# Optimization experiments

Hardware: AMD Instinct MI355X
Metric: run time of the kernel (lower is better)

## Reference

```python
import jax, jax.numpy as jnp
import numpy as np
from functools import partial

INPUT_DIM = 256
HIDDEN = 512
NUM_LAYERS = 2

def _linp(key, fan_in, shape):
    # torch nn.Linear/Conv default init: U(-1/sqrt(fan_in), 1/sqrt(fan_in))
    bound = 1.0 / np.sqrt(fan_in)
    return jax.random.uniform(key, shape, jnp.float32, -bound, bound)

def setup_inputs() -> dict:
    key = jax.random.key(0)
    ks = iter(jax.random.split(key, 64))
    d = {}
    d["x"] = jax.random.normal(next(ks), (32, 16, 1, 64, 64), jnp.float32)
    # encoder convs (OIHW)
    d["conv1_w"] = _linp(next(ks), 1 * 9, (16, 1, 3, 3));   d["conv1_b"] = _linp(next(ks), 1 * 9, (16,))
    d["conv2_w"] = _linp(next(ks), 16 * 9, (32, 16, 3, 3)); d["conv2_b"] = _linp(next(ks), 16 * 9, (32,))
    d["conv3_w"] = _linp(next(ks), 32 * 9, (INPUT_DIM, 32, 3, 3)); d["conv3_b"] = _linp(next(ks), 32 * 9, (INPUT_DIM,))
    # LSTM cells: per layer 4 gate linears (forget, input, cell, output), in = input+hidden
    for j in range(NUM_LAYERS):
        fan = (INPUT_DIM if j == 0 else HIDDEN) + HIDDEN
        for g in ("f", "i", "g", "o"):
            d[f"W{g}{j}"] = _linp(next(ks), fan, (fan, HIDDEN))
            d[f"b{g}{j}"] = _linp(next(ks), fan, (HIDDEN,))
    # classifier
    d["cw1"] = _linp(next(ks), HIDDEN, (HIDDEN, 128)); d["cb1"] = _linp(next(ks), HIDDEN, (128,))
    d["cw2"] = _linp(next(ks), 128, (128, 64));        d["cb2"] = _linp(next(ks), 128, (64,))
    d["cw3"] = _linp(next(ks), 64, (64, 6));           d["cb3"] = _linp(next(ks), 64, (6,))
    return d

def _conv(x, w, b):
    y = jax.lax.conv_general_dilated(x, w, (1, 1), "SAME",
                                     dimension_numbers=("NCHW", "OIHW", "NCHW"))
    return y + b[None, :, None, None]

def _maxpool2(x):
    return jax.lax.reduce_window(x, -jnp.inf, jax.lax.max,
                                 (1, 1, 2, 2), (1, 1, 2, 2), "VALID")

def reference(x, conv1_w, conv1_b, conv2_w, conv2_b, conv3_w, conv3_b,
              Wf0, bf0, Wi0, bi0, Wg0, bg0, Wo0, bo0,
              Wf1, bf1, Wi1, bi1, Wg1, bg1, Wo1, bo1,
              cw1, cb1, cw2, cb2, cw3, cb3):
    B, T, C, H, W = x.shape
    xf = x.reshape(B * T, C, H, W)
    h = _maxpool2(jax.nn.relu(_conv(xf, conv1_w, conv1_b)))
    h = _maxpool2(jax.nn.relu(_conv(h, conv2_w, conv2_b)))
    h = jax.nn.relu(_conv(h, conv3_w, conv3_b))
    emb = h.mean(axis=(2, 3)).reshape(B, T, -1)  # AdaptiveAvgPool2d((1,1)); dropout = identity (eval)

    layers = [(Wf0, bf0, Wi0, bi0, Wg0, bg0, Wo0, bo0),
              (Wf1, bf1, Wi1, bi1, Wg1, bg1, Wo1, bo1)]

    def step(carry, x_t):
        hs, cs = carry
        inp = x_t
        new_h, new_c = [], []
        for j, (Wf, bf, Wi, bi, Wg, bg, Wo, bo) in enumerate(layers):
            comb = jnp.concatenate([inp, hs[j]], axis=1)  # [B, in+H]
            f_t = jax.nn.sigmoid(comb @ Wf + bf)
            i_t = jax.nn.sigmoid(comb @ Wi + bi)
            g_t = jnp.tanh(comb @ Wg + bg)
            o_t = jax.nn.sigmoid(comb @ Wo + bo)
            c_n = f_t * cs[j] + i_t * g_t
            h_n = o_t * jnp.tanh(c_n)
            new_h.append(h_n); new_c.append(c_n)
            inp = h_n
        return (tuple(new_h), tuple(new_c)), None

    h0 = tuple(jnp.zeros((B, HIDDEN), x.dtype) for _ in range(NUM_LAYERS))
    c0 = tuple(jnp.zeros((B, HIDDEN), x.dtype) for _ in range(NUM_LAYERS))
    (hs, _), _ = jax.lax.scan(step, (h0, c0), jnp.swapaxes(emb, 0, 1))
    last = hs[-1]  # [B, HIDDEN], last timestep top-layer h (dropout = identity)

    y = jax.nn.relu(last @ cw1 + cb1)
    y = jax.nn.relu(y @ cw2 + cb2)
    return y @ cw3 + cb3  # [B, 6]
```

## Files before the change

### kernel.cpp

```cpp
#include <hip/hip_runtime.h>
#include <math.h>

__global__ void k_conv1(const float* __restrict__ x, const float* __restrict__ w,
                        const float* __restrict__ bias, float* __restrict__ out) {
  int idx = blockIdx.x * 256 + threadIdx.x;
  int ox = idx & 31, oy = (idx >> 5) & 31, oc = (idx >> 10) & 15, n = idx >> 14;
  const float* im = x + n * 4096;
  float wv[9];
#pragma unroll
  for (int i = 0; i < 9; ++i) wv[i] = w[oc * 9 + i];
  float bs = bias[oc];
  float m = 0.f;
#pragma unroll
  for (int dy = 0; dy < 2; ++dy)
#pragma unroll
    for (int dx = 0; dx < 2; ++dx) {
      int cy = oy * 2 + dy, cx = ox * 2 + dx;
      float s = bs;
#pragma unroll
      for (int ky = 0; ky < 3; ++ky) {
        int yy = cy + ky - 1;
        if (yy < 0 || yy >= 64) continue;
#pragma unroll
        for (int kx = 0; kx < 3; ++kx) {
          int xx = cx + kx - 1;
          if (xx < 0 || xx >= 64) continue;
          s += im[yy * 64 + xx] * wv[ky * 3 + kx];
        }
      }
      m = fmaxf(m, fmaxf(s, 0.f));
    }
  out[idx] = m;
}

__global__ void k_prep_w(const float* __restrict__ w2, float* __restrict__ w2t,
                         const float* __restrict__ w3, float* __restrict__ w3t) {
  int id = blockIdx.x * 256 + threadIdx.x;
  if (id < 73728) {
    int ct = id >> 8, oc = id & 255;
    int c = ct / 9, tap = ct - 9 * c;
    w3t[id] = w3[(oc * 32 + c) * 9 + tap];
  }
  if (id < 4608) {
    int ct = id >> 5, oc = id & 31;
    int c = ct / 9, tap = ct - 9 * c;
    w2t[id] = w2[(oc * 16 + c) * 9 + tap];
  }
}

__global__ __launch_bounds__(256) void k_conv2(
    const float* __restrict__ a1, const float* __restrict__ w2t,
    const float* __restrict__ bias, float* __restrict__ a2) {
  __shared__ __align__(16) float ins[8 * 1024];
  int n = blockIdx.x, ocg = blockIdx.y;
  int tid = threadIdx.x;
  int py = tid >> 4, px = tid & 15;
  int y0 = 2 * py - 1, x0 = 2 * px - 1;
  float acc[16][4] = {};
  const float* wb = w2t + ocg * 16;
  for (int ph = 0; ph < 2; ++ph) {
    __syncthreads();
    const float4* src = (const float4*)(a1 + n * 16384 + ph * 8192);
    for (int i = tid; i < 2048; i += 256) ((float4*)ins)[i] = src[i];
    __syncthreads();
    for (int c = 0; c < 8; ++c) {
      float wv[4][4];
#pragma unroll
      for (int r = 0; r < 4; ++r) {
        int y = y0 + r;
        bool vy = (y >= 0) && (y < 32);
        int yc = vy ? y : 0;
#pragma unroll
        for (int cc = 0; cc < 4; ++cc) {
          int xx = x0 + cc;
          bool vx = (xx >= 0) && (xx < 32);
          int xc = vx ? xx : 0;
          float t = ins[c * 1024 + yc * 32 + xc];
          wv[r][cc] = (vy && vx) ? t : 0.f;
        }
      }
      int ch = ph * 8 + c;
#pragma unroll
      for (int ky = 0; ky < 3; ++ky)
#pragma unroll
        for (int kx = 0; kx < 3; ++kx) {
          const float* w16 = wb + (ch * 9 + ky * 3 + kx) * 32;
#pragma unroll
          for (int i = 0; i < 4; ++i) {
            float vv = wv[(i >> 1) + ky][(i & 1) + kx];
#pragma unroll
            for (int j = 0; j < 16; ++j) acc[j][i] += vv * w16[j];
          }
        }
    }
  }
  const float* bp = bias + ocg * 16;
  float4 o[4];
#pragma unroll
  for (int j = 0; j < 16; ++j) {
    float m = fmaxf(fmaxf(acc[j][0], acc[j][1]), fmaxf(acc[j][2], acc[j][3]));
    ((float*)o)[j] = fmaxf(m + bp[j], 0.f);
  }
  float4* dst = (float4*)(a2 + (size_t)(n * 256 + tid) * 32 + ocg * 16);
#pragma unroll
  for (int q = 0; q < 4; ++q) dst[q] = o[q];
}

__global__ __launch_bounds__(512, 4) void k_conv3(
    const float* __restrict__ a2, const float* __restrict__ w3t,
    const float* __restrict__ bias, float* __restrict__ comb0) {
  __shared__ __align__(16) float ins[324 * 20];
  float4* ins4 = (float4*)ins;
  int n = blockIdx.x, ocb = blockIdx.y;
  int tid = threadIdx.x;
  for (int i = tid; i < 1620; i += 512) ins4[i] = float4{0.f, 0.f, 0.f, 0.f};
  int wvid = __builtin_amdgcn_readfirstlane(tid >> 6);
  int lane = tid & 63;
  int tr = lane >> 4, tc = lane & 15;
  float acc[4][16] = {};
  const float* wbase = w3t + ocb * 128 + wvid * 16;
  const float4* src = (const float4*)(a2 + (size_t)n * 8192);
  for (int hf = 0; hf < 2; ++hf) {
    __syncthreads();
    for (int i = tid; i < 1024; i += 512) {
      int px = i >> 2, cg = i & 3;
      int p = ((px >> 4) + 1) * 18 + (px & 15) + 1;
      ins4[p * 5 + cg] = src[px * 8 + hf * 4 + cg];
    }
    __syncthreads();
    for (int cg = 0; cg < 4; ++cg) {
      int chb = hf * 16 + cg * 4;
#pragma unroll
      for (int dr = 0; dr < 6; ++dr) {
#pragma unroll
        for (int dc = 0; dc < 3; ++dc) {
          int pp = (4 * tr + dr) * 18 + tc + dc;
          float4 v = ins4[pp * 5 + cg];
#pragma unroll
          for (int c = 0; c < 4; ++c) {
            float vv = ((const float*)&v)[c];
            const int ilo = (dr - 2 < 0) ? 0 : dr - 2;
            const int ihi = (dr < 3) ? dr : 3;
#pragma unroll
            for (int i = ilo; i <= ihi; ++i) {
              const float* w16 = wbase + (((chb + c) * 9 + (dr - i) * 3 + dc) * 256);
#pragma unroll
              for (int j = 0; j < 16; ++j) acc[i][j] += vv * w16[j];
            }
          }
        }
      }
    }
  }
  const float* bp = bias + ocb * 128 + wvid * 16;
  int bb = n >> 4, tt = n & 15;
#pragma unroll
  for (int j = 0; j < 16; ++j) {
    float bj = bp[j];
    float s = 0.f;
#pragma unroll
    for (int i = 0; i < 4; ++i) s += fmaxf(acc[i][j] + bj, 0.f);
#pragma unroll
    for (int off = 32; off; off >>= 1) s += __shfl_down(s, off, 64);
    if (lane == 0) {
      int oc = ocb * 128 + wvid * 16 + j;
      comb0[(size_t)(tt * 768 + oc) * 32 + bb] = s * (1.f / 256.f);
    }
  }
}

struct TPtrs { const float* in[8]; float* out[8]; };

__global__ void k_transpose(TPtrs p) {
  __shared__ float tile[32][33];
  int z = blockIdx.z;
  int fan = (z < 4) ? 768 : 1024;
  int k0 = blockIdx.x * 32, h0 = blockIdx.y * 32;
  if (k0 >= fan) return;
  const float* in = p.in[z];
  float* out = p.out[z];
  int tx = threadIdx.x, ty = threadIdx.y;
  for (int r = 0; r < 32; r += 8)
    tile[ty + r][tx] = in[(k0 + ty + r) * 512 + h0 + tx];
  __syncthreads();
  for (int r = 0; r < 32; r += 8)
    out[(h0 + ty + r) * fan + k0 + tx] = tile[tx][ty + r];
}

struct LstmArgs {
  const float* comb; float* houtA; float* houtB; float* cT;
  const float* Wf; const float* Wi; const float* Wg; const float* Wo;
  const float* bf; const float* bi; const float* bg; const float* bo;
};

template <int IN>
__device__ __forceinline__ void lstm_body(int h, int tid, const LstmArgs& A,
                                          float* wl, float* gsum, float* pre) {
  constexpr int FAN = IN + 512;
  constexpr int PR = FAN + 4;
  constexpr int KT = FAN / 16;
  if (tid < FAN / 4) {
    ((float4*)(wl + 0 * PR))[tid] = ((const float4*)(A.Wf + (size_t)h * FAN))[tid];
    ((float4*)(wl + 1 * PR))[tid] = ((const float4*)(A.Wi + (size_t)h * FAN))[tid];
    ((float4*)(wl + 2 * PR))[tid] = ((const float4*)(A.Wg + (size_t)h * FAN))[tid];
    ((float4*)(wl + 3 * PR))[tid] = ((const float4*)(A.Wo + (size_t)h * FAN))[tid];
  }
  __syncthreads();
  const int kq = (tid >> 3) & 15, c = tid >> 7, bq = tid & 7;
  const int kbase = kq * KT;
  const float4* w4 = (const float4*)(wl + c * PR + kbase);
  const float4* a4 = (const float4*)A.comb + bq;
  float acc0 = 0.f, acc1 = 0.f, acc2 = 0.f, acc3 = 0.f;
#pragma unroll
  for (int kk = 0; kk < KT / 4; ++kk) {
    float4 w = w4[kk];
#pragma unroll
    for (int j = 0; j < 4; ++j) {
      float wj = ((const float*)&w)[j];
      float4 a = a4[(size_t)(kbase + kk * 4 + j) * 8];
      acc0 += wj * a.x; acc1 += wj * a.y; acc2 += wj * a.z; acc3 += wj * a.w;
    }
  }
  ((float4*)(gsum + (c * 16 + kq) * 36))[bq] = float4{acc0, acc1, acc2, acc3};
  __syncthreads();
  if (tid < 128) {
    int cc = tid >> 5, b = tid & 31;
    float s = 0.f;
#pragma unroll
    for (int q = 0; q < 16; ++q) s += gsum[(cc * 16 + q) * 36 + b];
    pre[cc * 33 + b] = s;
  }
  __syncthreads();
  if (tid < 32) {
    int b = tid;
    float fp = pre[0 * 33 + b] + A.bf[h];
    float ip = pre[1 * 33 + b] + A.bi[h];
    float gp = pre[2 * 33 + b] + A.bg[h];
    float op = pre[3 * 33 + b] + A.bo[h];
    float ft = 1.f / (1.f + expf(-fp));
    float it = 1.f / (1.f + expf(-ip));
    float gt = tanhf(gp);
    float ot = 1.f / (1.f + expf(-op));
    float cn = ft * A.cT[h * 32 + b] + it * gt;
    A.cT[h * 32 + b] = cn;
    float hn = ot * tanhf(cn);
    A.houtA[h * 32 + b] = hn;
    A.houtB[h * 32 + b] = hn;
  }
}

template <int IN>
__global__ __launch_bounds__(512) void k_lstm(LstmArgs a) {
  __shared__ __align__(16) float wl[4 * 1028];
  __shared__ __align__(16) float gsum[4 * 16 * 36];
  __shared__ float pre[4 * 33];
  lstm_body<IN>(blockIdx.x, threadIdx.x, a, wl, gsum, pre);
}

__global__ __launch_bounds__(512) void k_lstm_pair(LstmArgs a0, LstmArgs a1) {
  __shared__ __align__(16) float wl[4 * 1028];
  __shared__ __align__(16) float gsum[4 * 16 * 36];
  __shared__ float pre[4 * 33];
  if (blockIdx.x < 512)
    lstm_body<256>(blockIdx.x, threadIdx.x, a0, wl, gsum, pre);
  else
    lstm_body<512>(blockIdx.x - 512, threadIdx.x, a1, wl, gsum, pre);
}

__global__ void k_cls(const float* __restrict__ h1T, const float* __restrict__ cw1,
                      const float* __restrict__ cb1, const float* __restrict__ cw2,
                      const float* __restrict__ cb2, const float* __restrict__ cw3,
                      const float* __restrict__ cb3, float* __restrict__ out) {
  __shared__ float hv[512];
  __shared__ float y1[128];
  __shared__ float y2[64];
  int b = blockIdx.x, tid = threadIdx.x;
  for (int i = tid; i < 512; i += 128) hv[i] = h1T[i * 32 + b];
  __syncthreads();
  float s = cb1[tid];
  for (int k = 0; k < 512; ++k) s += hv[k] * cw1[k * 128 + tid];
  y1[tid] = fmaxf(s, 0.f);
  __syncthreads();
  if (tid < 64) {
    float s2 = cb2[tid];
    for (int k = 0; k < 128; ++k) s2 += y1[k] * cw2[k * 64 + tid];
    y2[tid] = fmaxf(s2, 0.f);
  }
  __syncthreads();
  if (tid < 6) {
    float s3 = cb3[tid];
    for (int k = 0; k < 64; ++k) s3 += y2[k] * cw3[k * 6 + tid];
    out[b * 6 + tid] = s3;
  }
}

extern "C" void kernel_launch(void* const* d_in, const int* in_sizes, int n_in,
                              void* d_out, int out_size, void* d_ws, size_t ws_size,
                              hipStream_t stream) {
  const float* x  = (const float*)d_in[0];
  const float* w1 = (const float*)d_in[1];
  const float* b1 = (const float*)d_in[2];
  const float* w2 = (const float*)d_in[3];
  const float* b2 = (const float*)d_in[4];
  const float* w3 = (const float*)d_in[5];
  const float* b3 = (const float*)d_in[6];
  const float* cw1 = (const float*)d_in[23];
  const float* cb1 = (const float*)d_in[24];
  const float* cw2 = (const float*)d_in[25];
  const float* cb2 = (const float*)d_in[26];
  const float* cw3 = (const float*)d_in[27];
  const float* cb3 = (const float*)d_in[28];

  float* ws = (float*)d_ws;
  float* a1    = ws;
  float* wt    = ws;
  float* comb0 = ws + 3670016;
  float* comb1 = ws + 4087808;
  float* c0    = ws + 4644864;
  float* c1    = ws + 4661248;
  float* a2    = ws + 8388608;
  float* w2t   = ws + 12582912;
  float* w3t   = ws + 12587520;
  const int C0 = 768 * 32, C1 = 1024 * 32;

  k_prep_w<<<288, 256, 0, stream>>>(w2, w2t, w3, w3t);
  k_conv1<<<32768, 256, 0, stream>>>(x, w1, b1, a1);
  k_conv2<<<dim3(512, 2), 256, 0, stream>>>(a1, w2t, b2, a2);

  hipMemsetAsync(comb0 + 256 * 32, 0, (size_t)512 * 32 * 4, stream);
  hipMemsetAsync(comb1 + 512 * 32, 0, (size_t)512 * 32 * 4, stream);
  hipMemsetAsync(c0, 0, (size_t)2 * 512 * 32 * 4, stream);

  k_conv3<<<dim3(512, 2), 512, 0, stream>>>(a2, w3t, b3, comb0);

  TPtrs tp;
  for (int g = 0; g < 4; ++g) {
    tp.in[g]      = (const float*)d_in[7 + 2 * g];
    tp.out[g]     = wt + g * (512 * 768);
    tp.in[4 + g]  = (const float*)d_in[15 + 2 * g];
    tp.out[4 + g] = wt + 4 * (512 * 768) + g * (512 * 1024);
  }
  k_transpose<<<dim3(32, 16, 8), dim3(32, 8), 0, stream>>>(tp);

  const float* wl0[4] = {wt, wt + 393216, wt + 786432, wt + 1179648};
  float* l1base = wt + 1572864;
  const float* wl1[4] = {l1base, l1base + 524288, l1base + 1048576, l1base + 1572864};

  auto L0 = [&](int t) {
    LstmArgs a;
    a.comb = comb0 + (size_t)t * C0;
    a.houtA = comb0 + (size_t)(t + 1) * C0 + 256 * 32;
    a.houtB = comb1 + (size_t)t * C1;
    a.cT = c0;
    a.Wf = wl0[0]; a.Wi = wl0[1]; a.Wg = wl0[2]; a.Wo = wl0[3];
    a.bf = (const float*)d_in[8];  a.bi = (const float*)d_in[10];
    a.bg = (const float*)d_in[12]; a.bo = (const float*)d_in[14];
    return a;
  };
  auto L1 = [&](int t) {
    LstmArgs a;
    a.comb = comb1 + (size_t)t * C1;
    a.houtA = comb1 + (size_t)(t + 1) * C1 + 512 * 32;
    a.houtB = a.houtA;
    a.cT = c1;
    a.Wf = wl1[0]; a.Wi = wl1[1]; a.Wg = wl1[2]; a.Wo = wl1[3];
    a.bf = (const float*)d_in[16]; a.bi = (const float*)d_in[18];
    a.bg = (const float*)d_in[20]; a.bo = (const float*)d_in[22];
    return a;
  };

  k_lstm<256><<<512, 512, 0, stream>>>(L0(0));
  for (int p = 0; p < 15; ++p)
    k_lstm_pair<<<1024, 512, 0, stream>>>(L0(p + 1), L1(p));
  k_lstm<512><<<512, 512, 0, stream>>>(L1(15));

  k_cls<<<32, 128, 0, stream>>>(comb1 + (size_t)16 * C1 + 512 * 32,
                                cw1, cb1, cw2, cb2, cw3, cb3, (float*)d_out);
}
```

Before: 687.6 us.

## Retile conv3 to 8 channels per wave and pack LSTM gate weights interleaved

conv3 now runs 256-thread blocks with 8 output channels per wave across 8 channel-block groups. It preloads an 6x3 float4 input window into registers and loops over kernel taps, in place of the earlier per-row accumulate pattern. The LSTM gate weights are packed into one interleaved float4 layout (f,i,g,o per k), so each step kernel streams weights straight from global memory without staging them in LDS. Each wave then reduces a K-slice for all 32 batch lanes with a cross-half shuffle. This aims to cut shared-memory staging and synchronisation per LSTM step and to raise conv3 occupancy, at the cost of more redundant input loads across the extra conv3 blocks.

```diff
diff --git a/kernel.cpp b/kernel.cpp
--- a/kernel.cpp
+++ b/kernel.cpp
@@ -106,56 +106,54 @@
   for (int q = 0; q < 4; ++q) dst[q] = o[q];
 }
 
-__global__ __launch_bounds__(512, 4) void k_conv3(
+__global__ __launch_bounds__(256) void k_conv3(
     const float* __restrict__ a2, const float* __restrict__ w3t,
     const float* __restrict__ bias, float* __restrict__ comb0) {
   __shared__ __align__(16) float ins[324 * 20];
-  float4* ins4 = (float4*)ins;
   int n = blockIdx.x, ocb = blockIdx.y;
   int tid = threadIdx.x;
-  for (int i = tid; i < 1620; i += 512) ins4[i] = float4{0.f, 0.f, 0.f, 0.f};
+  for (int i = tid; i < 1620; i += 256) ((float4*)ins)[i] = float4{0.f, 0.f, 0.f, 0.f};
   int wvid = __builtin_amdgcn_readfirstlane(tid >> 6);
   int lane = tid & 63;
   int tr = lane >> 4, tc = lane & 15;
-  float acc[4][16] = {};
-  const float* wbase = w3t + ocb * 128 + wvid * 16;
+  float acc[4][8] = {};
+  const float* wbase = w3t + ocb * 32 + wvid * 8;
   const float4* src = (const float4*)(a2 + (size_t)n * 8192);
   for (int hf = 0; hf < 2; ++hf) {
     __syncthreads();
-    for (int i = tid; i < 1024; i += 512) {
+    for (int i = tid; i < 1024; i += 256) {
       int px = i >> 2, cg = i & 3;
       int p = ((px >> 4) + 1) * 18 + (px & 15) + 1;
-      ins4[p * 5 + cg] = src[px * 8 + hf * 4 + cg];
+      ((float4*)ins)[p * 5 + cg] = src[px * 8 + hf * 4 + cg];
     }
     __syncthreads();
     for (int cg = 0; cg < 4; ++cg) {
-      int chb = hf * 16 + cg * 4;
-#pragma unroll
-      for (int dr = 0; dr < 6; ++dr) {
-#pragma unroll
-        for (int dc = 0; dc < 3; ++dc) {
-          int pp = (4 * tr + dr) * 18 + tc + dc;
-          float4 v = ins4[pp * 5 + cg];
+      float4 v[6][3];
+#pragma unroll
+      for (int dr = 0; dr < 6; ++dr)
+#pragma unroll
+        for (int dc = 0; dc < 3; ++dc)
+          v[dr][dc] = ((const float4*)ins)[((4 * tr + dr) * 18 + tc + dc) * 5 + cg];
+#pragma unroll
+      for (int ky = 0; ky < 3; ++ky)
+#pragma unroll
+        for (int kx = 0; kx < 3; ++kx)
 #pragma unroll
           for (int c = 0; c < 4; ++c) {
-            float vv = ((const float*)&v)[c];
-            const int ilo = (dr - 2 < 0) ? 0 : dr - 2;
-            const int ihi = (dr < 3) ? dr : 3;
-#pragma unroll
-            for (int i = ilo; i <= ihi; ++i) {
-              const float* w16 = wbase + (((chb + c) * 9 + (dr - i) * 3 + dc) * 256);
-#pragma unroll
-              for (int j = 0; j < 16; ++j) acc[i][j] += vv * w16[j];
+            const float* w8 = wbase + (((hf * 4 + cg) * 4 + c) * 9 + ky * 3 + kx) * 256;
+#pragma unroll
+            for (int i = 0; i < 4; ++i) {
+              float vv = ((const float*)&v[i + ky][kx])[c];
+#pragma unroll
+              for (int j = 0; j < 8; ++j) acc[i][j] += vv * w8[j];
             }
           }
-        }
-      }
-    }
-  }
-  const float* bp = bias + ocb * 128 + wvid * 16;
+    }
+  }
+  const float* bp = bias + ocb * 32 + wvid * 8;
   int bb = n >> 4, tt = n & 15;
 #pragma unroll
-  for (int j = 0; j < 16; ++j) {
+  for (int j = 0; j < 8; ++j) {
     float bj = bp[j];
     float s = 0.f;
 #pragma unroll
@@ -163,108 +161,105 @@
 #pragma unroll
     for (int off = 32; off; off >>= 1) s += __shfl_down(s, off, 64);
     if (lane == 0) {
-      int oc = ocb * 128 + wvid * 16 + j;
+      int oc = ocb * 32 + wvid * 8 + j;
       comb0[(size_t)(tt * 768 + oc) * 32 + bb] = s * (1.f / 256.f);
     }
   }
 }
 
-struct TPtrs { const float* in[8]; float* out[8]; };
-
-__global__ void k_transpose(TPtrs p) {
-  __shared__ float tile[32][33];
-  int z = blockIdx.z;
-  int fan = (z < 4) ? 768 : 1024;
+__global__ void k_pack(const float* __restrict__ Wf, const float* __restrict__ Wi,
+                       const float* __restrict__ Wg, const float* __restrict__ Wo,
+                       float* __restrict__ p, int fan) {
+  __shared__ float t[4][32][33];
   int k0 = blockIdx.x * 32, h0 = blockIdx.y * 32;
-  if (k0 >= fan) return;
-  const float* in = p.in[z];
-  float* out = p.out[z];
-  int tx = threadIdx.x, ty = threadIdx.y;
-  for (int r = 0; r < 32; r += 8)
-    tile[ty + r][tx] = in[(k0 + ty + r) * 512 + h0 + tx];
-  __syncthreads();
-  for (int r = 0; r < 32; r += 8)
-    out[(h0 + ty + r) * fan + k0 + tx] = tile[tx][ty + r];
-}
-
-struct LstmArgs {
-  const float* comb; float* houtA; float* houtB; float* cT;
-  const float* Wf; const float* Wi; const float* Wg; const float* Wo;
+  int tx = threadIdx.x & 31, ty = threadIdx.x >> 5;
+  const float* Ws[4] = {Wf, Wi, Wg, Wo};
+#pragma unroll
+  for (int g = 0; g < 4; ++g)
+    for (int r = 0; r < 32; r += 8)
+      t[g][ty + r][tx] = Ws[g][(size_t)(k0 + ty + r) * 512 + h0 + tx];
+  __syncthreads();
+  for (int r = 0; r < 32; r += 8) {
+    int hh = ty + r;
+    float4 v = {t[0][tx][hh], t[1][tx][hh], t[2][tx][hh], t[3][tx][hh]};
+    ((float4*)p)[(size_t)(h0 + hh) * fan + k0 + tx] = v;
+  }
+}
+
+struct SArgs {
+  const float* comb;
+  const float* pw;
+  float* houtA; float* houtB; float* cT;
   const float* bf; const float* bi; const float* bg; const float* bo;
 };
 
-template <int IN>
-__device__ __forceinline__ void lstm_body(int h, int tid, const LstmArgs& A,
-                                          float* wl, float* gsum, float* pre) {
-  constexpr int FAN = IN + 512;
-  constexpr int PR = FAN + 4;
-  constexpr int KT = FAN / 16;
-  if (tid < FAN / 4) {
-    ((float4*)(wl + 0 * PR))[tid] = ((const float4*)(A.Wf + (size_t)h * FAN))[tid];
-    ((float4*)(wl + 1 * PR))[tid] = ((const float4*)(A.Wi + (size_t)h * FAN))[tid];
-    ((float4*)(wl + 2 * PR))[tid] = ((const float4*)(A.Wg + (size_t)h * FAN))[tid];
-    ((float4*)(wl + 3 * PR))[tid] = ((const float4*)(A.Wo + (size_t)h * FAN))[tid];
-  }
-  __syncthreads();
-  const int kq = (tid >> 3) & 15, c = tid >> 7, bq = tid & 7;
-  const int kbase = kq * KT;
-  const float4* w4 = (const float4*)(wl + c * PR + kbase);
-  const float4* a4 = (const float4*)A.comb + bq;
-  float acc0 = 0.f, acc1 = 0.f, acc2 = 0.f, acc3 = 0.f;
-#pragma unroll
-  for (int kk = 0; kk < KT / 4; ++kk) {
-    float4 w = w4[kk];
-#pragma unroll
-    for (int j = 0; j < 4; ++j) {
-      float wj = ((const float*)&w)[j];
-      float4 a = a4[(size_t)(kbase + kk * 4 + j) * 8];
-      acc0 += wj * a.x; acc1 += wj * a.y; acc2 += wj * a.z; acc3 += wj * a.w;
-    }
-  }
-  ((float4*)(gsum + (c * 16 + kq) * 36))[bq] = float4{acc0, acc1, acc2, acc3};
-  __syncthreads();
-  if (tid < 128) {
-    int cc = tid >> 5, b = tid & 31;
-    float s = 0.f;
-#pragma unroll
-    for (int q = 0; q < 16; ++q) s += gsum[(cc * 16 + q) * 36 + b];
-    pre[cc * 33 + b] = s;
+template <int FAN>
+__device__ __forceinline__ void lstm_sbody(int h, int tid, const SArgs& A,
+                                           float* __restrict__ gsum) {
+  constexpr int CH = FAN / 8;
+  const int wv = __builtin_amdgcn_readfirstlane(tid >> 6);
+  const int lane = tid & 63;
+  const int ks = lane >> 5, b = lane & 31;
+  const int kb = wv * CH;
+  const float4* pw4 = (const float4*)A.pw + (size_t)h * FAN + kb;
+  const float* ac = A.comb + (size_t)kb * 32 + lane;
+  float a0 = 0.f, a1 = 0.f, a2 = 0.f, a3 = 0.f;
+#pragma unroll 8
+  for (int kk = 0; kk < CH; kk += 2) {
+    float4 w0 = pw4[kk];
+    float4 w1 = pw4[kk + 1];
+    float av = ac[kk * 32];
+    a0 += av * (ks ? w1.x : w0.x);
+    a1 += av * (ks ? w1.y : w0.y);
+    a2 += av * (ks ? w1.z : w0.z);
+    a3 += av * (ks ? w1.w : w0.w);
+  }
+  a0 += __shfl_xor(a0, 32);
+  a1 += __shfl_xor(a1, 32);
+  a2 += __shfl_xor(a2, 32);
+  a3 += __shfl_xor(a3, 32);
+  if (lane < 32) {
+    gsum[(wv * 4 + 0) * 33 + b] = a0;
+    gsum[(wv * 4 + 1) * 33 + b] = a1;
+    gsum[(wv * 4 + 2) * 33 + b] = a2;
+    gsum[(wv * 4 + 3) * 33 + b] = a3;
   }
   __syncthreads();
   if (tid < 32) {
-    int b = tid;
-    float fp = pre[0 * 33 + b] + A.bf[h];
-    float ip = pre[1 * 33 + b] + A.bi[h];
-    float gp = pre[2 * 33 + b] + A.bg[h];
-    float op = pre[3 * 33 + b] + A.bo[h];
+    float fp = A.bf[h], ip = A.bi[h], gp = A.bg[h], op = A.bo[h];
+#pragma unroll
+    for (int q = 0; q < 8; ++q) {
+      fp += gsum[(q * 4 + 0) * 33 + tid];
+      ip += gsum[(q * 4 + 1) * 33 + tid];
+      gp += gsum[(q * 4 + 2) * 33 + tid];
+      op += gsum[(q * 4 + 3) * 33 + tid];
+    }
     float ft = 1.f / (1.f + expf(-fp));
-    float it = 1.f / (1.f + expf(-ip));
+    float it_ = 1.f / (1.f + expf(-ip));
     float gt = tanhf(gp);
     float ot = 1.f / (1.f + expf(-op));
-    float cn = ft * A.cT[h * 32 + b] + it * gt;
-    A.cT[h * 32 + b] = cn;
+    float cn = ft * A.cT[h * 32 + tid] + it_ * gt;
+    A.cT[h * 32 + tid] = cn;
     float hn = ot * tanhf(cn);
-    A.houtA[h * 32 + b] = hn;
-    A.houtB[h * 32 + b] = hn;
-  }
-}
-
-template <int IN>
-__global__ __launch_bounds__(512) void k_lstm(LstmArgs a) {
-  __shared__ __align__(16) float wl[4 * 1028];
-  __shared__ __align__(16) float gsum[4 * 16 * 36];
-  __shared__ float pre[4 * 33];
-  lstm_body<IN>(blockIdx.x, threadIdx.x, a, wl, gsum, pre);
-}
-
-__global__ __launch_bounds__(512) void k_lstm_pair(LstmArgs a0, LstmArgs a1) {
-  __shared__ __align__(16) float wl[4 * 1028];
-  __shared__ __align__(16) float gsum[4 * 16 * 36];
-  __shared__ float pre[4 * 33];
+    A.houtA[h * 32 + tid] = hn;
+    A.houtB[h * 32 + tid] = hn;
+  }
+}
+
+__global__ __launch_bounds__(512) void k_lstm_s0(SArgs a) {
+  __shared__ float gsum[32 * 33];
+  lstm_sbody<768>(blockIdx.x, threadIdx.x, a, gsum);
+}
+__global__ __launch_bounds__(512) void k_lstm_s1(SArgs a) {
+  __shared__ float gsum[32 * 33];
+  lstm_sbody<1024>(blockIdx.x, threadIdx.x, a, gsum);
+}
+__global__ __launch_bounds__(512) void k_lstm_spair(SArgs a0, SArgs a1) {
+  __shared__ float gsum[32 * 33];
   if (blockIdx.x < 512)
-    lstm_body<256>(blockIdx.x, threadIdx.x, a0, wl, gsum, pre);
+    lstm_sbody<768>(blockIdx.x, threadIdx.x, a0, gsum);
   else
-    lstm_body<512>(blockIdx.x - 512, threadIdx.x, a1, wl, gsum, pre);
+    lstm_sbody<1024>(blockIdx.x - 512, threadIdx.x, a1, gsum);
 }
 
 __global__ void k_cls(const float* __restrict__ h1T, const float* __restrict__ cw1,
@@ -313,7 +308,8 @@
 
   float* ws = (float*)d_ws;
   float* a1    = ws;
-  float* wt    = ws;
+  float* p0    = ws;
+  float* p1    = ws + 1572864;
   float* comb0 = ws + 3670016;
   float* comb1 = ws + 4087808;
   float* c0    = ws + 4644864;
@@ -331,48 +327,42 @@
   hipMemsetAsync(comb1 + 512 * 32, 0, (size_t)512 * 32 * 4, stream);
   hipMemsetAsync(c0, 0, (size_t)2 * 512 * 32 * 4, stream);
 
-  k_conv3<<<dim3(512, 2), 512, 0, stream>>>(a2, w3t, b3, comb0);
-
-  TPtrs tp;
-  for (int g = 0; g < 4; ++g) {
-    tp.in[g]      = (const float*)d_in[7 + 2 * g];
-    tp.out[g]     = wt + g * (512 * 768);
-    tp.in[4 + g]  = (const float*)d_in[15 + 2 * g];
-    tp.out[4 + g] = wt + 4 * (512 * 768) + g * (512 * 1024);
-  }
-  k_transpose<<<dim3(32, 16, 8), dim3(32, 8), 0, stream>>>(tp);
-
-  const float* wl0[4] = {wt, wt + 393216, wt + 786432, wt + 1179648};
-  float* l1base = wt + 1572864;
-  const float* wl1[4] = {l1base, l1base + 524288, l1base + 1048576, l1base + 1572864};
+  k_conv3<<<dim3(512, 8), 256, 0, stream>>>(a2, w3t, b3, comb0);
+
+  k_pack<<<dim3(24, 16), 256, 0, stream>>>(
+      (const float*)d_in[7], (const float*)d_in[9],
+      (const float*)d_in[11], (const float*)d_in[13], p0, 768);
+  k_pack<<<dim3(32, 16), 256, 0, stream>>>(
+      (const float*)d_in[15], (const float*)d_in[17],
+      (const float*)d_in[19], (const float*)d_in[21], p1, 1024);
 
   auto L0 = [&](int t) {
-    LstmArgs a;
+    SArgs a;
     a.comb = comb0 + (size_t)t * C0;
+    a.pw = p0;
     a.houtA = comb0 + (size_t)(t + 1) * C0 + 256 * 32;
     a.houtB = comb1 + (size_t)t * C1;
     a.cT = c0;
-    a.Wf = wl0[0]; a.Wi = wl0[1]; a.Wg = wl0[2]; a.Wo = wl0[3];
     a.bf = (const float*)d_in[8];  a.bi = (const float*)d_in[10];
     a.bg = (const float*)d_in[12]; a.bo = (const float*)d_in[14];
     return a;
   };
   auto L1 = [&](int t) {
-    LstmArgs a;
+    SArgs a;
     a.comb = comb1 + (size_t)t * C1;
+    a.pw = p1;
     a.houtA = comb1 + (size_t)(t + 1) * C1 + 512 * 32;
     a.houtB = a.houtA;
     a.cT = c1;
-    a.Wf = wl1[0]; a.Wi = wl1[1]; a.Wg = wl1[2]; a.Wo = wl1[3];
     a.bf = (const float*)d_in[16]; a.bi = (const float*)d_in[18];
     a.bg = (const float*)d_in[20]; a.bo = (const float*)d_in[22];
     return a;
   };
 
-  k_lstm<256><<<512, 512, 0, stream>>>(L0(0));
+  k_lstm_s0<<<512, 512, 0, stream>>>(L0(0));
   for (int p = 0; p < 15; ++p)
-    k_lstm_pair<<<1024, 512, 0, stream>>>(L0(p + 1), L1(p));
-  k_lstm<512><<<512, 512, 0, stream>>>(L1(15));
+    k_lstm_spair<<<1024, 512, 0, stream>>>(L0(p + 1), L1(p));
+  k_lstm_s1<<<512, 512, 0, stream>>>(L1(15));
 
   k_cls<<<32, 128, 0, stream>>>(comb1 + (size_t)16 * C1 + 512 * 32,
                                 cw1, cb1, cw2, cb2, cw3, cb3, (float*)d_out);
```

Measured after the change: 687.9 us. Within noise of the previous version (+0.0%).
